# Optimization experiments

Measured on AMD Instinct MI355X. Metric: run time of the kernel, lower is better.

## Reference

```python
import jax, jax.numpy as jnp
import numpy as np

RADIUS = 1.0


def setup_inputs() -> dict:
    key = jax.random.key(0)
    ks = jax.random.split(key, 9)
    Nq, No, P, L = 1024, 2048, 3, 64
    pos_query = jax.random.uniform(ks[0], (Nq, P), dtype=jnp.float32)
    pos_obs = jax.random.uniform(ks[1], (No, P), dtype=jnp.float32)
    h_obs = jax.random.normal(ks[2], (No, L), dtype=jnp.float32)
    # kernel_mlp: Linear(3*P, L) -> ReLU -> Linear(L, 1)
    W1 = jax.random.normal(ks[3], (3 * P, L), dtype=jnp.float32) * (1.0 / np.sqrt(3 * P))
    b1 = jnp.zeros((L,), jnp.float32)
    W2 = jax.random.normal(ks[4], (L, 1), dtype=jnp.float32) * (1.0 / np.sqrt(L))
    b2 = jnp.zeros((1,), jnp.float32)
    # value_proj: Linear(L, L)
    Wv = jax.random.normal(ks[5], (L, L), dtype=jnp.float32) * (1.0 / np.sqrt(L))
    bv = jnp.zeros((L,), jnp.float32)
    obs_mask = jnp.ones((No,), jnp.int32)
    obs_batch = jnp.sort(jax.random.randint(ks[6], (No,), 0, 4, dtype=jnp.int32))
    query_batch = jnp.sort(jax.random.randint(ks[7], (Nq,), 0, 4, dtype=jnp.int32))
    return dict(h_obs=h_obs, pos_obs=pos_obs, pos_query=pos_query,
                W1=W1, b1=b1, W2=W2, b2=b2, Wv=Wv, bv=bv,
                obs_mask=obs_mask, obs_batch=obs_batch, query_batch=query_batch)


def reference(h_obs, pos_obs, pos_query, W1, b1, W2, b2, Wv, bv,
              obs_mask, obs_batch, query_batch):
    Nq, P = pos_query.shape
    No = pos_obs.shape[0]
    rel = pos_query[:, None, :] - pos_obs[None, :, :]                 # [Nq,No,P]
    kin = jnp.concatenate([
        jnp.broadcast_to(pos_query[:, None, :], (Nq, No, P)),
        jnp.broadcast_to(pos_obs[None, :, :], (Nq, No, P)),
        rel,
    ], axis=-1)                                                        # [Nq,No,3P]
    hidden = jax.nn.relu(jnp.einsum('qop,pl->qol', kin, W1) + b1)      # [Nq,No,L]
    logits = jnp.einsum('qol,lk->qok', hidden, W2)[..., 0] + b2[0]     # [Nq,No]
    # masks: same batch, within radius, observed
    same = query_batch[:, None] == obs_batch[None, :]
    dist = jnp.linalg.norm(rel, axis=-1)
    mask = same & (dist <= RADIUS) & (obs_mask[None, :] != 0)
    # masked softmax over obs dim; fully-masked rows -> all-zero weights
    # (matches torch softmax(-inf row) -> nan -> nan_to_num(0))
    logits_safe = jnp.where(mask, logits, 0.0)
    m = jnp.max(jnp.where(mask, logits, -jnp.inf), axis=1, keepdims=True)
    m = jnp.where(jnp.isfinite(m), m, 0.0)
    e = jnp.where(mask, jnp.exp(logits_safe - m), 0.0)
    denom = jnp.sum(e, axis=1, keepdims=True)
    weights = e / jnp.maximum(denom, 1e-30)                            # [Nq,No]
    v = h_obs @ Wv + bv                                                # [No,L]
    return weights @ v                                                 # [Nq,L]
```

## Files before the change

kernel.cpp:

```cpp
#include <hip/hip_runtime.h>
#include <math.h>

#define LDIM 64
#define QT2 32
#define QW 8
#define LOG2E 1.4426950408889634f

static __device__ __forceinline__ float fast_exp2(float x) {
#if __has_builtin(__builtin_amdgcn_exp2f)
    return __builtin_amdgcn_exp2f(x);
#else
    return exp2f(x);
#endif
}

__global__ __launch_bounds__(256) void gano_pre(
    const float* __restrict__ h_obs, const float* __restrict__ pos_obs,
    const float* __restrict__ pos_query,
    const float* __restrict__ W1, const float* __restrict__ b1,
    const float* __restrict__ W2,
    const float* __restrict__ Wv, const float* __restrict__ bv,
    const int* __restrict__ obs_mask, const int* __restrict__ obs_batch,
    float4* __restrict__ Bi, float4* __restrict__ P4, float* __restrict__ V,
    float* __restrict__ A, float* __restrict__ w2s, float* __restrict__ zeroRegion,
    int No, int NoA, int Nq)
{
    const int gid = blockIdx.x * blockDim.x + threadIdx.x;
    if (gid >= NoA * LDIM) return;
    {
        const int o = gid >> 6, l = gid & 63;
        float vv = 0.0f;
        if (o < No) {
            vv = bv[l];
            #pragma unroll 16
            for (int k = 0; k < LDIM; ++k)
                vv = fmaf(h_obs[o * LDIM + k], Wv[k * LDIM + l], vv);
        }
        V[gid] = vv;
    }
    if (gid < NoA * 16) {
        const int o = gid & 63, g = (gid >> 6) & 15, c = gid >> 10;
        const int oo = (c << 6) + o;
        float4 r = make_float4(0.f, 0.f, 0.f, 0.f);
        if (oo < No) {
            const float px = pos_obs[oo*3+0], py = pos_obs[oo*3+1], pz = pos_obs[oo*3+2];
            float* rr = (float*)&r;
            #pragma unroll
            for (int j = 0; j < 4; ++j) {
                const int l = 4 * g + j;
                float bb = b1[l];
                bb = fmaf(px, W1[3*LDIM+l] - W1[6*LDIM+l], bb);
                bb = fmaf(py, W1[4*LDIM+l] - W1[7*LDIM+l], bb);
                bb = fmaf(pz, W1[5*LDIM+l] - W1[8*LDIM+l], bb);
                rr[j] = bb;
            }
        }
        Bi[gid] = r;
    }
    if (gid < Nq * LDIM) {
        const int q = gid >> 6, l = gid & 63;
        float a = pos_query[q*3+0] * (W1[0*LDIM+l] + W1[6*LDIM+l]);
        a = fmaf(pos_query[q*3+1], W1[1*LDIM+l] + W1[7*LDIM+l], a);
        a = fmaf(pos_query[q*3+2], W1[2*LDIM+l] + W1[8*LDIM+l], a);
        A[gid] = a;
    }
    if (gid < LDIM) w2s[gid] = W2[gid] * LOG2E;
    if (gid < NoA) {
        float4 pp = make_float4(0.f, 0.f, 0.f, 0.f);
        if (gid < No)
            pp = make_float4(pos_obs[gid*3+0], pos_obs[gid*3+1], pos_obs[gid*3+2],
                             obs_mask[gid] ? (float)(obs_batch[gid] + 1) : 0.0f);
        P4[gid] = pp;
    }
    if (gid < Nq * (LDIM + 1)) zeroRegion[gid] = 0.0f;
}

__global__ __launch_bounds__(256) void gano_accum(
    const float4* __restrict__ Bi, const float4* __restrict__ P4,
    const float* __restrict__ V, const float* __restrict__ A,
    const float* __restrict__ w2s, const float* __restrict__ pos_query,
    const int* __restrict__ obs_batch, const int* __restrict__ query_batch,
    float* __restrict__ acc, float* __restrict__ den,
    int No, int Nq)
{
    const int c  = blockIdx.x;
    const int q0 = blockIdx.y * QT2;
    if ((c << 6) >= No) return;
    const int c_lo = obs_batch[c << 6];
    const int c_hi = obs_batch[min((c << 6) + 63, No - 1)];
    if (c_lo > query_batch[q0 + QT2 - 1] || c_hi < query_batch[q0]) return;

    __shared__ float4 a4[QT2][16];
    __shared__ float4 w2_4[16];
    __shared__ float4 qp4[QT2];
    __shared__ float  e_lds[QT2][LDIM];

    const int tid = threadIdx.x;
    for (int i = tid; i < QT2 * 16; i += 256)
        a4[i >> 4][i & 15] = ((const float4*)A)[((size_t)(q0 + (i >> 4)) << 4) + (i & 15)];
    if (tid < 16) w2_4[tid] = ((const float4*)w2s)[tid];
    if (tid < QT2) {
        const int q = q0 + tid;
        qp4[tid] = make_float4(pos_query[q*3+0], pos_query[q*3+1], pos_query[q*3+2],
                               (float)(query_batch[q] + 1));
    }
    __syncthreads();

    const int lane = tid & 63, wid = tid >> 6;
    const float4 p = P4[(c << 6) + lane];
    const float4* Bc = Bi + ((size_t)c << 10) + lane;

    float lgq[QW];
    #pragma unroll
    for (int j = 0; j < QW; ++j) lgq[j] = 0.0f;
    #pragma unroll
    for (int g = 0; g < 16; ++g) {
        const float4 Bv = Bc[g << 6];
        const float4 w  = w2_4[g];
        #pragma unroll
        for (int j = 0; j < QW; ++j) {
            const float4 a = a4[wid * QW + j][g];
            lgq[j] = fmaf(fmaxf(a.x + Bv.x, 0.f), w.x, lgq[j]);
            lgq[j] = fmaf(fmaxf(a.y + Bv.y, 0.f), w.y, lgq[j]);
            lgq[j] = fmaf(fmaxf(a.z + Bv.z, 0.f), w.z, lgq[j]);
            lgq[j] = fmaf(fmaxf(a.w + Bv.w, 0.f), w.w, lgq[j]);
        }
    }

    float ds[QW];
    #pragma unroll
    for (int j = 0; j < QW; ++j) {
        const float4 qp = qp4[wid * QW + j];
        const float dx = qp.x - p.x, dy = qp.y - p.y, dz = qp.z - p.z;
        const float d2 = fmaf(dz, dz, fmaf(dy, dy, dx * dx));
        const bool valid = (p.w == qp.w) & (d2 <= 1.0f);
        const float e = valid ? fast_exp2(lgq[j]) : 0.0f;
        e_lds[wid * QW + j][lane] = e;
        ds[j] = e;
    }
    #pragma unroll
    for (int msk = 32; msk; msk >>= 1) {
        #pragma unroll
        for (int j = 0; j < QW; ++j) ds[j] += __shfl_xor(ds[j], msk, 64);
    }
    if (lane == 0) {
        #pragma unroll
        for (int j = 0; j < QW; ++j) atomicAdd(&den[q0 + wid * QW + j], ds[j]);
    }

    const float* Vc = V + ((size_t)c << 12) + lane;
    float pacc[QW];
    #pragma unroll
    for (int j = 0; j < QW; ++j) pacc[j] = 0.0f;
    for (int oo = 0; oo < LDIM; oo += 4) {
        const float v0 = Vc[(oo + 0) << 6];
        const float v1 = Vc[(oo + 1) << 6];
        const float v2 = Vc[(oo + 2) << 6];
        const float v3 = Vc[(oo + 3) << 6];
        #pragma unroll
        for (int j = 0; j < QW; ++j) {
            const float4 e = *(const float4*)&e_lds[wid * QW + j][oo];
            pacc[j] = fmaf(e.x, v0, pacc[j]);
            pacc[j] = fmaf(e.y, v1, pacc[j]);
            pacc[j] = fmaf(e.z, v2, pacc[j]);
            pacc[j] = fmaf(e.w, v3, pacc[j]);
        }
    }
    #pragma unroll
    for (int j = 0; j < QW; ++j)
        atomicAdd(&acc[(size_t)(q0 + wid * QW + j) * LDIM + lane], pacc[j]);
}

__global__ __launch_bounds__(256) void gano_norm(
    const float* __restrict__ acc, const float* __restrict__ den,
    float* __restrict__ out, int n)
{
    const int gid = blockIdx.x * blockDim.x + threadIdx.x;
    if (gid >= n) return;
    out[gid] = acc[gid] / fmaxf(den[gid >> 6], 1e-30f);
}

extern "C" void kernel_launch(void* const* d_in, const int* in_sizes, int n_in,
                              void* d_out, int out_size, void* d_ws, size_t ws_size,
                              hipStream_t stream) {
    const float* h_obs     = (const float*)d_in[0];
    const float* pos_obs   = (const float*)d_in[1];
    const float* pos_query = (const float*)d_in[2];
    const float* W1        = (const float*)d_in[3];
    const float* b1        = (const float*)d_in[4];
    const float* W2        = (const float*)d_in[5];
    const float* Wv        = (const float*)d_in[7];
    const float* bv        = (const float*)d_in[8];
    const int* obs_mask    = (const int*)d_in[9];
    const int* obs_batch   = (const int*)d_in[10];
    const int* query_batch = (const int*)d_in[11];

    const int No  = in_sizes[1] / 3;
    const int Nq  = in_sizes[2] / 3;
    const int NoA = (No + 63) & ~63;
    const int nC  = NoA / 64;

    float4* Bi  = (float4*)d_ws;
    float4* P4  = Bi + (size_t)NoA * 16;
    float*  V   = (float*)(P4 + NoA);
    float*  A   = V + (size_t)NoA * LDIM;
    float*  w2s = A + (size_t)Nq * LDIM;
    float*  acc = w2s + LDIM;
    float*  den = acc + (size_t)Nq * LDIM;

    gano_pre<<<(NoA * LDIM + 255) / 256, 256, 0, stream>>>(
        h_obs, pos_obs, pos_query, W1, b1, W2, Wv, bv, obs_mask, obs_batch,
        Bi, P4, V, A, w2s, acc, No, NoA, Nq);

    dim3 g2(nC, Nq / QT2);
    gano_accum<<<g2, 256, 0, stream>>>(Bi, P4, V, A, w2s, pos_query,
                                       obs_batch, query_batch, acc, den, No, Nq);

    gano_norm<<<(Nq * LDIM + 255) / 256, 256, 0, stream>>>(acc, den, (float*)d_out, Nq * LDIM);
}
```

Baseline: 29.04 us.

## Fuse first-layer projections and normalization into accumulation kernel with last-block finalize

Moves the per-query and per-observation first-layer projections out of the pre-kernel and computes them in LDS inside the accumulation kernel. The separate normalization kernel is replaced by a per-tile arrival counter: the last block to finish a query tile divides the accumulators by the denominator. Active chunk ranges are found by binary search over the sorted batch ids. This removes one launch and the global round trips for the intermediate buffers, at the cost of redundant projection work per block plus a fence and atomic counter per block.

```diff
diff --git a/kernel.cpp b/kernel.cpp
--- a/kernel.cpp
+++ b/kernel.cpp
@@ -14,108 +14,126 @@
 #endif
 }
 
+static __device__ __forceinline__ float4 ld4(const float* p) {
+    return *(const float4*)p;
+}
+
 __global__ __launch_bounds__(256) void gano_pre(
-    const float* __restrict__ h_obs, const float* __restrict__ pos_obs,
-    const float* __restrict__ pos_query,
-    const float* __restrict__ W1, const float* __restrict__ b1,
-    const float* __restrict__ W2,
-    const float* __restrict__ Wv, const float* __restrict__ bv,
-    const int* __restrict__ obs_mask, const int* __restrict__ obs_batch,
-    float4* __restrict__ Bi, float4* __restrict__ P4, float* __restrict__ V,
-    float* __restrict__ A, float* __restrict__ w2s, float* __restrict__ zeroRegion,
-    int No, int NoA, int Nq)
+    const float* __restrict__ h_obs, const float* __restrict__ Wv,
+    const float* __restrict__ bv,
+    float* __restrict__ V, float* __restrict__ zeroRegion,
+    int No, int NoA, int zn)
 {
     const int gid = blockIdx.x * blockDim.x + threadIdx.x;
     if (gid >= NoA * LDIM) return;
-    {
-        const int o = gid >> 6, l = gid & 63;
-        float vv = 0.0f;
-        if (o < No) {
-            vv = bv[l];
-            #pragma unroll 16
-            for (int k = 0; k < LDIM; ++k)
-                vv = fmaf(h_obs[o * LDIM + k], Wv[k * LDIM + l], vv);
-        }
-        V[gid] = vv;
-    }
-    if (gid < NoA * 16) {
-        const int o = gid & 63, g = (gid >> 6) & 15, c = gid >> 10;
-        const int oo = (c << 6) + o;
-        float4 r = make_float4(0.f, 0.f, 0.f, 0.f);
-        if (oo < No) {
-            const float px = pos_obs[oo*3+0], py = pos_obs[oo*3+1], pz = pos_obs[oo*3+2];
-            float* rr = (float*)&r;
-            #pragma unroll
-            for (int j = 0; j < 4; ++j) {
-                const int l = 4 * g + j;
-                float bb = b1[l];
-                bb = fmaf(px, W1[3*LDIM+l] - W1[6*LDIM+l], bb);
-                bb = fmaf(py, W1[4*LDIM+l] - W1[7*LDIM+l], bb);
-                bb = fmaf(pz, W1[5*LDIM+l] - W1[8*LDIM+l], bb);
-                rr[j] = bb;
+    const int o = gid >> 6, l = gid & 63;
+    float vv = 0.0f;
+    if (o < No) {
+        vv = bv[l];
+        #pragma unroll 16
+        for (int k = 0; k < LDIM; ++k)
+            vv = fmaf(h_obs[o * LDIM + k], Wv[k * LDIM + l], vv);
+    }
+    V[gid] = vv;
+    if (gid < zn) zeroRegion[gid] = 0.0f;
+}
+
+__global__ __launch_bounds__(256) void gano_fused(
+    const float* __restrict__ pos_obs, const float* __restrict__ pos_query,
+    const float* __restrict__ W1, const float* __restrict__ b1,
+    const float* __restrict__ W2, const float* __restrict__ V,
+    const int* __restrict__ obs_mask, const int* __restrict__ obs_batch,
+    const int* __restrict__ query_batch,
+    float* __restrict__ acc, float* __restrict__ den, int* __restrict__ cnt,
+    float* __restrict__ out, int No, int Nq, int nC)
+{
+    const int c   = blockIdx.x;
+    const int t   = blockIdx.y;
+    const int q0  = t * QT2;
+    const int tid = threadIdx.x, lane = tid & 63, wid = tid >> 6;
+
+    const int t_lo = query_batch[q0];
+    const int t_hi = query_batch[min(q0 + QT2 - 1, Nq - 1)];
+
+    int lo = 0, hi = nC;
+    while (lo < hi) { int mid = (lo + hi) >> 1;
+        if (obs_batch[min(mid * 64 + 63, No - 1)] < t_lo) lo = mid + 1; else hi = mid; }
+    const int cs = lo;
+    lo = 0; hi = nC;
+    while (lo < hi) { int mid = (lo + hi) >> 1;
+        if (obs_batch[mid * 64] <= t_hi) lo = mid + 1; else hi = mid; }
+    const int ce = lo - 1;
+    const int expected = (ce >= cs) ? (ce - cs + 1) : 0;
+    const bool active = (c >= cs) & (c <= ce);
+
+    if (!active) {
+        if (c == 0 && expected == 0) {
+            for (int i = tid; i < QT2 * LDIM; i += 256) {
+                const int q = q0 + (i >> 6);
+                if (q < Nq) out[(size_t)q * LDIM + (i & 63)] = 0.0f;
             }
         }
-        Bi[gid] = r;
-    }
-    if (gid < Nq * LDIM) {
-        const int q = gid >> 6, l = gid & 63;
-        float a = pos_query[q*3+0] * (W1[0*LDIM+l] + W1[6*LDIM+l]);
-        a = fmaf(pos_query[q*3+1], W1[1*LDIM+l] + W1[7*LDIM+l], a);
-        a = fmaf(pos_query[q*3+2], W1[2*LDIM+l] + W1[8*LDIM+l], a);
-        A[gid] = a;
-    }
-    if (gid < LDIM) w2s[gid] = W2[gid] * LOG2E;
-    if (gid < NoA) {
-        float4 pp = make_float4(0.f, 0.f, 0.f, 0.f);
-        if (gid < No)
-            pp = make_float4(pos_obs[gid*3+0], pos_obs[gid*3+1], pos_obs[gid*3+2],
-                             obs_mask[gid] ? (float)(obs_batch[gid] + 1) : 0.0f);
-        P4[gid] = pp;
-    }
-    if (gid < Nq * (LDIM + 1)) zeroRegion[gid] = 0.0f;
-}
-
-__global__ __launch_bounds__(256) void gano_accum(
-    const float4* __restrict__ Bi, const float4* __restrict__ P4,
-    const float* __restrict__ V, const float* __restrict__ A,
-    const float* __restrict__ w2s, const float* __restrict__ pos_query,
-    const int* __restrict__ obs_batch, const int* __restrict__ query_batch,
-    float* __restrict__ acc, float* __restrict__ den,
-    int No, int Nq)
-{
-    const int c  = blockIdx.x;
-    const int q0 = blockIdx.y * QT2;
-    if ((c << 6) >= No) return;
-    const int c_lo = obs_batch[c << 6];
-    const int c_hi = obs_batch[min((c << 6) + 63, No - 1)];
-    if (c_lo > query_batch[q0 + QT2 - 1] || c_hi < query_batch[q0]) return;
-
+        return;
+    }
+
+    __shared__ float4 B4[16][64];
     __shared__ float4 a4[QT2][16];
     __shared__ float4 w2_4[16];
     __shared__ float4 qp4[QT2];
     __shared__ float  e_lds[QT2][LDIM];
-
-    const int tid = threadIdx.x;
-    for (int i = tid; i < QT2 * 16; i += 256)
-        a4[i >> 4][i & 15] = ((const float4*)A)[((size_t)(q0 + (i >> 4)) << 4) + (i & 15)];
-    if (tid < 16) w2_4[tid] = ((const float4*)w2s)[tid];
+    __shared__ int    sLast;
+
     if (tid < QT2) {
-        const int q = q0 + tid;
+        const int q = min(q0 + tid, Nq - 1);
         qp4[tid] = make_float4(pos_query[q*3+0], pos_query[q*3+1], pos_query[q*3+2],
                                (float)(query_batch[q] + 1));
     }
+    if (tid < 16) {
+        const float4 w = ld4(W2 + 4 * tid);
+        w2_4[tid] = make_float4(w.x * LOG2E, w.y * LOG2E, w.z * LOG2E, w.w * LOG2E);
+    }
+    for (int i = tid; i < QT2 * 16; i += 256) {
+        const int q = i >> 4, g = i & 15;
+        const int qq = min(q0 + q, Nq - 1);
+        const float px = pos_query[qq*3+0], py = pos_query[qq*3+1], pz = pos_query[qq*3+2];
+        const float4 u0 = ld4(W1 + 0*LDIM + 4*g), u6 = ld4(W1 + 6*LDIM + 4*g);
+        const float4 u1 = ld4(W1 + 1*LDIM + 4*g), u7 = ld4(W1 + 7*LDIM + 4*g);
+        const float4 u2 = ld4(W1 + 2*LDIM + 4*g), u8 = ld4(W1 + 8*LDIM + 4*g);
+        float4 r;
+        r.x = fmaf(px, u0.x+u6.x, fmaf(py, u1.x+u7.x, pz*(u2.x+u8.x)));
+        r.y = fmaf(px, u0.y+u6.y, fmaf(py, u1.y+u7.y, pz*(u2.y+u8.y)));
+        r.z = fmaf(px, u0.z+u6.z, fmaf(py, u1.z+u7.z, pz*(u2.z+u8.z)));
+        r.w = fmaf(px, u0.w+u6.w, fmaf(py, u1.w+u7.w, pz*(u2.w+u8.w)));
+        a4[q][g] = r;
+    }
+    const int oo = (c << 6) + lane;
+    float px = 0.f, py = 0.f, pz = 0.f, pcode = 0.f;
+    if (oo < No) {
+        px = pos_obs[oo*3+0]; py = pos_obs[oo*3+1]; pz = pos_obs[oo*3+2];
+        pcode = obs_mask[oo] ? (float)(obs_batch[oo] + 1) : 0.0f;
+    }
+    #pragma unroll
+    for (int k = 0; k < 4; ++k) {
+        const int g = ((tid >> 6) + k * 4) & 15;
+        const float4 b0 = ld4(b1 + 4*g);
+        const float4 u3 = ld4(W1 + 3*LDIM + 4*g), u6 = ld4(W1 + 6*LDIM + 4*g);
+        const float4 u4 = ld4(W1 + 4*LDIM + 4*g), u7 = ld4(W1 + 7*LDIM + 4*g);
+        const float4 u5 = ld4(W1 + 5*LDIM + 4*g), u8 = ld4(W1 + 8*LDIM + 4*g);
+        float4 r;
+        r.x = fmaf(px, u3.x-u6.x, fmaf(py, u4.x-u7.x, fmaf(pz, u5.x-u8.x, b0.x)));
+        r.y = fmaf(px, u3.y-u6.y, fmaf(py, u4.y-u7.y, fmaf(pz, u5.y-u8.y, b0.y)));
+        r.z = fmaf(px, u3.z-u6.z, fmaf(py, u4.z-u7.z, fmaf(pz, u5.z-u8.z, b0.z)));
+        r.w = fmaf(px, u3.w-u6.w, fmaf(py, u4.w-u7.w, fmaf(pz, u5.w-u8.w, b0.w)));
+        B4[g][lane] = r;
+    }
     __syncthreads();
 
-    const int lane = tid & 63, wid = tid >> 6;
-    const float4 p = P4[(c << 6) + lane];
-    const float4* Bc = Bi + ((size_t)c << 10) + lane;
-
     float lgq[QW];
     #pragma unroll
     for (int j = 0; j < QW; ++j) lgq[j] = 0.0f;
     #pragma unroll
     for (int g = 0; g < 16; ++g) {
-        const float4 Bv = Bc[g << 6];
+        const float4 Bv = B4[g][lane];
         const float4 w  = w2_4[g];
         #pragma unroll
         for (int j = 0; j < QW; ++j) {
@@ -131,9 +149,9 @@
     #pragma unroll
     for (int j = 0; j < QW; ++j) {
         const float4 qp = qp4[wid * QW + j];
-        const float dx = qp.x - p.x, dy = qp.y - p.y, dz = qp.z - p.z;
+        const float dx = qp.x - px, dy = qp.y - py, dz = qp.z - pz;
         const float d2 = fmaf(dz, dz, fmaf(dy, dy, dx * dx));
-        const bool valid = (p.w == qp.w) & (d2 <= 1.0f);
+        const bool valid = (pcode == qp.w) & (d2 <= 1.0f);
         const float e = valid ? fast_exp2(lgq[j]) : 0.0f;
         e_lds[wid * QW + j][lane] = e;
         ds[j] = e;
@@ -152,14 +170,14 @@
     float pacc[QW];
     #pragma unroll
     for (int j = 0; j < QW; ++j) pacc[j] = 0.0f;
-    for (int oo = 0; oo < LDIM; oo += 4) {
-        const float v0 = Vc[(oo + 0) << 6];
-        const float v1 = Vc[(oo + 1) << 6];
-        const float v2 = Vc[(oo + 2) << 6];
-        const float v3 = Vc[(oo + 3) << 6];
+    for (int o2 = 0; o2 < LDIM; o2 += 4) {
+        const float v0 = Vc[(o2 + 0) << 6];
+        const float v1 = Vc[(o2 + 1) << 6];
+        const float v2 = Vc[(o2 + 2) << 6];
+        const float v3 = Vc[(o2 + 3) << 6];
         #pragma unroll
         for (int j = 0; j < QW; ++j) {
-            const float4 e = *(const float4*)&e_lds[wid * QW + j][oo];
+            const float4 e = *(const float4*)&e_lds[wid * QW + j][o2];
             pacc[j] = fmaf(e.x, v0, pacc[j]);
             pacc[j] = fmaf(e.y, v1, pacc[j]);
             pacc[j] = fmaf(e.z, v2, pacc[j]);
@@ -169,15 +187,28 @@
     #pragma unroll
     for (int j = 0; j < QW; ++j)
         atomicAdd(&acc[(size_t)(q0 + wid * QW + j) * LDIM + lane], pacc[j]);
-}
-
-__global__ __launch_bounds__(256) void gano_norm(
-    const float* __restrict__ acc, const float* __restrict__ den,
-    float* __restrict__ out, int n)
-{
-    const int gid = blockIdx.x * blockDim.x + threadIdx.x;
-    if (gid >= n) return;
-    out[gid] = acc[gid] / fmaxf(den[gid >> 6], 1e-30f);
+
+    __threadfence();
+    __syncthreads();
+    if (tid == 0) {
+        const int old = __hip_atomic_fetch_add(&cnt[t], 1, __ATOMIC_ACQ_REL,
+                                               __HIP_MEMORY_SCOPE_AGENT);
+        sLast = (old == expected - 1);
+    }
+    __syncthreads();
+    if (sLast) {
+        for (int i = tid; i < QT2 * LDIM; i += 256) {
+            const int q = q0 + (i >> 6);
+            if (q < Nq) {
+                const float D = __hip_atomic_load(&den[q], __ATOMIC_RELAXED,
+                                                  __HIP_MEMORY_SCOPE_AGENT);
+                const float Av = __hip_atomic_load(&acc[(size_t)q * LDIM + (i & 63)],
+                                                   __ATOMIC_RELAXED,
+                                                   __HIP_MEMORY_SCOPE_AGENT);
+                out[(size_t)q * LDIM + (i & 63)] = Av / fmaxf(D, 1e-30f);
+            }
+        }
+    }
 }
 
 extern "C" void kernel_launch(void* const* d_in, const int* in_sizes, int n_in,
@@ -195,26 +226,24 @@
     const int* obs_batch   = (const int*)d_in[10];
     const int* query_batch = (const int*)d_in[11];
 
-    const int No  = in_sizes[1] / 3;
-    const int Nq  = in_sizes[2] / 3;
-    const int NoA = (No + 63) & ~63;
-    const int nC  = NoA / 64;
-
-    float4* Bi  = (float4*)d_ws;
-    float4* P4  = Bi + (size_t)NoA * 16;
-    float*  V   = (float*)(P4 + NoA);
-    float*  A   = V + (size_t)NoA * LDIM;
-    float*  w2s = A + (size_t)Nq * LDIM;
-    float*  acc = w2s + LDIM;
-    float*  den = acc + (size_t)Nq * LDIM;
+    const int No     = in_sizes[1] / 3;
+    const int Nq     = in_sizes[2] / 3;
+    const int NoA    = (No + 63) & ~63;
+    const int nC     = NoA / 64;
+    const int nTiles = (Nq + QT2 - 1) / QT2;
+
+    float* V   = (float*)d_ws;
+    float* acc = V + (size_t)NoA * LDIM;
+    float* den = acc + (size_t)Nq * LDIM;
+    int*   cnt = (int*)(den + Nq);
+    const int zn = Nq * (LDIM + 1) + nTiles;
 
     gano_pre<<<(NoA * LDIM + 255) / 256, 256, 0, stream>>>(
-        h_obs, pos_obs, pos_query, W1, b1, W2, Wv, bv, obs_mask, obs_batch,
-        Bi, P4, V, A, w2s, acc, No, NoA, Nq);
-
-    dim3 g2(nC, Nq / QT2);
-    gano_accum<<<g2, 256, 0, stream>>>(Bi, P4, V, A, w2s, pos_query,
-                                       obs_batch, query_batch, acc, den, No, Nq);
-
-    gano_norm<<<(Nq * LDIM + 255) / 256, 256, 0, stream>>>(acc, den, (float*)d_out, Nq * LDIM);
-}
+        h_obs, Wv, bv, V, acc, No, NoA, zn);
+
+    dim3 g2(nC, nTiles);
+    gano_fused<<<g2, 256, 0, stream>>>(
+        pos_obs, pos_query, W1, b1, W2, V,
+        obs_mask, obs_batch, query_batch,
+        acc, den, cnt, (float*)d_out, No, Nq, nC);
+}
```

After: 56.27 us. 1.94x slower.

## Apply value projection after attention aggregation instead of projecting every observation

Applied to the files above, without the earlier changes.

Uses linearity of the softmax-weighted sum to accumulate weights times raw h_obs, then applies Wv and bv once per query in the normalization kernel. This removes the No x L x L projection from the pre-kernel and the V workspace round-trip, and shrinks the pre-kernel grid. The change relies on the weights summing to one for non-empty rows so the bias is added only when den>0. It also adds tail-safe paths for partial observation chunks and partial query tiles.

```diff
diff --git a/kernel.cpp b/kernel.cpp
--- a/kernel.cpp
+++ b/kernel.cpp
@@ -14,30 +14,21 @@
 #endif
 }
 
+static __device__ __forceinline__ float4 ld4(const float* p) {
+    return *(const float4*)p;
+}
+
 __global__ __launch_bounds__(256) void gano_pre(
-    const float* __restrict__ h_obs, const float* __restrict__ pos_obs,
-    const float* __restrict__ pos_query,
+    const float* __restrict__ pos_obs, const float* __restrict__ pos_query,
     const float* __restrict__ W1, const float* __restrict__ b1,
     const float* __restrict__ W2,
-    const float* __restrict__ Wv, const float* __restrict__ bv,
     const int* __restrict__ obs_mask, const int* __restrict__ obs_batch,
-    float4* __restrict__ Bi, float4* __restrict__ P4, float* __restrict__ V,
-    float* __restrict__ A, float* __restrict__ w2s, float* __restrict__ zeroRegion,
-    int No, int NoA, int Nq)
+    float4* __restrict__ Bi, float4* __restrict__ P4,
+    float* __restrict__ A, float* __restrict__ w2s, float* __restrict__ zeroR,
+    int No, int NoA, int Nq, int zn)
 {
     const int gid = blockIdx.x * blockDim.x + threadIdx.x;
-    if (gid >= NoA * LDIM) return;
-    {
-        const int o = gid >> 6, l = gid & 63;
-        float vv = 0.0f;
-        if (o < No) {
-            vv = bv[l];
-            #pragma unroll 16
-            for (int k = 0; k < LDIM; ++k)
-                vv = fmaf(h_obs[o * LDIM + k], Wv[k * LDIM + l], vv);
-        }
-        V[gid] = vv;
-    }
+
     if (gid < NoA * 16) {
         const int o = gid & 63, g = (gid >> 6) & 15, c = gid >> 10;
         const int oo = (c << 6) + o;
@@ -72,12 +63,12 @@
                              obs_mask[gid] ? (float)(obs_batch[gid] + 1) : 0.0f);
         P4[gid] = pp;
     }
-    if (gid < Nq * (LDIM + 1)) zeroRegion[gid] = 0.0f;
+    if (gid < zn) zeroR[gid] = 0.0f;
 }
 
 __global__ __launch_bounds__(256) void gano_accum(
     const float4* __restrict__ Bi, const float4* __restrict__ P4,
-    const float* __restrict__ V, const float* __restrict__ A,
+    const float* __restrict__ h_obs, const float* __restrict__ A,
     const float* __restrict__ w2s, const float* __restrict__ pos_query,
     const int* __restrict__ obs_batch, const int* __restrict__ query_batch,
     float* __restrict__ acc, float* __restrict__ den,
@@ -88,7 +79,7 @@
     if ((c << 6) >= No) return;
     const int c_lo = obs_batch[c << 6];
     const int c_hi = obs_batch[min((c << 6) + 63, No - 1)];
-    if (c_lo > query_batch[q0 + QT2 - 1] || c_hi < query_batch[q0]) return;
+    if (c_lo > query_batch[min(q0 + QT2 - 1, Nq - 1)] || c_hi < query_batch[q0]) return;
 
     __shared__ float4 a4[QT2][16];
     __shared__ float4 w2_4[16];
@@ -100,7 +91,7 @@
         a4[i >> 4][i & 15] = ((const float4*)A)[((size_t)(q0 + (i >> 4)) << 4) + (i & 15)];
     if (tid < 16) w2_4[tid] = ((const float4*)w2s)[tid];
     if (tid < QT2) {
-        const int q = q0 + tid;
+        const int q = min(q0 + tid, Nq - 1);
         qp4[tid] = make_float4(pos_query[q*3+0], pos_query[q*3+1], pos_query[q*3+2],
                                (float)(query_batch[q] + 1));
     }
@@ -148,22 +139,32 @@
         for (int j = 0; j < QW; ++j) atomicAdd(&den[q0 + wid * QW + j], ds[j]);
     }
 
-    const float* Vc = V + ((size_t)c << 12) + lane;
+    const float* Hc = h_obs + ((size_t)c << 12) + lane;
     float pacc[QW];
     #pragma unroll
     for (int j = 0; j < QW; ++j) pacc[j] = 0.0f;
-    for (int oo = 0; oo < LDIM; oo += 4) {
-        const float v0 = Vc[(oo + 0) << 6];
-        const float v1 = Vc[(oo + 1) << 6];
-        const float v2 = Vc[(oo + 2) << 6];
-        const float v3 = Vc[(oo + 3) << 6];
-        #pragma unroll
-        for (int j = 0; j < QW; ++j) {
-            const float4 e = *(const float4*)&e_lds[wid * QW + j][oo];
-            pacc[j] = fmaf(e.x, v0, pacc[j]);
-            pacc[j] = fmaf(e.y, v1, pacc[j]);
-            pacc[j] = fmaf(e.z, v2, pacc[j]);
-            pacc[j] = fmaf(e.w, v3, pacc[j]);
+    if ((c << 6) + 64 <= No) {
+        for (int oo = 0; oo < LDIM; oo += 4) {
+            const float v0 = Hc[(oo + 0) << 6];
+            const float v1 = Hc[(oo + 1) << 6];
+            const float v2 = Hc[(oo + 2) << 6];
+            const float v3 = Hc[(oo + 3) << 6];
+            #pragma unroll
+            for (int j = 0; j < QW; ++j) {
+                const float4 e = *(const float4*)&e_lds[wid * QW + j][oo];
+                pacc[j] = fmaf(e.x, v0, pacc[j]);
+                pacc[j] = fmaf(e.y, v1, pacc[j]);
+                pacc[j] = fmaf(e.z, v2, pacc[j]);
+                pacc[j] = fmaf(e.w, v3, pacc[j]);
+            }
+        }
+    } else {
+        for (int oo = 0; oo < LDIM; ++oo) {
+            const int orow = min((c << 6) + oo, No - 1);
+            const float v = h_obs[((size_t)orow << 6) + lane];
+            #pragma unroll
+            for (int j = 0; j < QW; ++j)
+                pacc[j] = fmaf(e_lds[wid * QW + j][oo], v, pacc[j]);
         }
     }
     #pragma unroll
@@ -173,11 +174,32 @@
 
 __global__ __launch_bounds__(256) void gano_norm(
     const float* __restrict__ acc, const float* __restrict__ den,
-    float* __restrict__ out, int n)
+    const float* __restrict__ Wv, const float* __restrict__ bv,
+    float* __restrict__ out, int Nq)
 {
-    const int gid = blockIdx.x * blockDim.x + threadIdx.x;
-    if (gid >= n) return;
-    out[gid] = acc[gid] / fmaxf(den[gid >> 6], 1e-30f);
+    const int tid = threadIdx.x, lane = tid & 63, wid = tid >> 6;
+    const int q0 = blockIdx.x * 8 + wid * 2;
+    if (q0 >= Nq) return;
+
+    __shared__ float r_lds[4][2][LDIM];
+
+    const float D0 = den[q0];
+    const float D1 = (q0 + 1 < Nq) ? den[q0 + 1] : 0.0f;
+    const float rd0 = (D0 > 0.0f) ? 1.0f / D0 : 0.0f;
+    const float rd1 = (D1 > 0.0f) ? 1.0f / D1 : 0.0f;
+    r_lds[wid][0][lane] = acc[(size_t)q0 * LDIM + lane] * rd0;
+    r_lds[wid][1][lane] = (q0 + 1 < Nq) ? acc[(size_t)(q0 + 1) * LDIM + lane] * rd1 : 0.0f;
+    float o0 = 0.f, o1 = 0.f;
+    #pragma unroll 8
+    for (int k = 0; k < LDIM; ++k) {
+        const float w = Wv[(k << 6) + lane];
+        o0 = fmaf(r_lds[wid][0][k], w, o0);
+        o1 = fmaf(r_lds[wid][1][k], w, o1);
+    }
+    const float b = bv[lane];
+    out[(size_t)q0 * LDIM + lane] = (D0 > 0.0f) ? o0 + b : 0.0f;
+    if (q0 + 1 < Nq)
+        out[(size_t)(q0 + 1) * LDIM + lane] = (D1 > 0.0f) ? o1 + b : 0.0f;
 }
 
 extern "C" void kernel_launch(void* const* d_in, const int* in_sizes, int n_in,
@@ -195,26 +217,31 @@
     const int* obs_batch   = (const int*)d_in[10];
     const int* query_batch = (const int*)d_in[11];
 
-    const int No  = in_sizes[1] / 3;
-    const int Nq  = in_sizes[2] / 3;
-    const int NoA = (No + 63) & ~63;
-    const int nC  = NoA / 64;
+    const int No     = in_sizes[1] / 3;
+    const int Nq     = in_sizes[2] / 3;
+    const int NoA    = (No + 63) & ~63;
+    const int nC     = NoA / 64;
+    const int nTiles = (Nq + QT2 - 1) / QT2;
+    const int zn     = Nq * (LDIM + 1);
 
     float4* Bi  = (float4*)d_ws;
     float4* P4  = Bi + (size_t)NoA * 16;
-    float*  V   = (float*)(P4 + NoA);
-    float*  A   = V + (size_t)NoA * LDIM;
+    float*  A   = (float*)(P4 + NoA);
     float*  w2s = A + (size_t)Nq * LDIM;
     float*  acc = w2s + LDIM;
     float*  den = acc + (size_t)Nq * LDIM;
 
-    gano_pre<<<(NoA * LDIM + 255) / 256, 256, 0, stream>>>(
-        h_obs, pos_obs, pos_query, W1, b1, W2, Wv, bv, obs_mask, obs_batch,
-        Bi, P4, V, A, w2s, acc, No, NoA, Nq);
-
-    dim3 g2(nC, Nq / QT2);
-    gano_accum<<<g2, 256, 0, stream>>>(Bi, P4, V, A, w2s, pos_query,
+    int gridN = NoA * 16;
+    if (Nq * LDIM > gridN) gridN = Nq * LDIM;
+    if (zn > gridN) gridN = zn;
+
+    gano_pre<<<(gridN + 255) / 256, 256, 0, stream>>>(
+        pos_obs, pos_query, W1, b1, W2, obs_mask, obs_batch,
+        Bi, P4, A, w2s, acc, No, NoA, Nq, zn);
+
+    dim3 g2(nC, nTiles);
+    gano_accum<<<g2, 256, 0, stream>>>(Bi, P4, h_obs, A, w2s, pos_query,
                                        obs_batch, query_batch, acc, den, No, Nq);
 
-    gano_norm<<<(Nq * LDIM + 255) / 256, 256, 0, stream>>>(acc, den, (float*)d_out, Nq * LDIM);
-}
+    gano_norm<<<(Nq + 7) / 8, 256, 0, stream>>>(acc, den, Wv, bv, (float*)d_out, Nq);
+}
```

After: 32.39 us. +11.6%, slower.
